# Kernel tuning notes

Measured on AMD Instinct MI355X. Metric: run time of the kernel, lower is better.

## Reference

```python
import jax, jax.numpy as jnp
import numpy as np

B, D, V, T = 256, 1024, 32000, 64  # num_seqs, hidden dim, vocab, history len


def setup_inputs() -> dict:
    key = jax.random.key(0)
    ks = jax.random.split(key, 8)
    hidden = jax.random.normal(ks[0], (B, D), dtype=jnp.float32)
    embedding = jax.random.normal(ks[1], (V, D), dtype=jnp.float32) * (1.0 / np.sqrt(D))
    output_tokens = jax.random.randint(ks[2], (B, T), 0, V, dtype=jnp.int64)
    presence_penalties = jax.random.uniform(ks[3], (B,), dtype=jnp.float32)
    frequency_penalties = jax.random.uniform(ks[4], (B,), dtype=jnp.float32)
    temperatures = jax.random.uniform(ks[5], (B,), dtype=jnp.float32) + 0.5  # > eps
    top_ps = jax.random.uniform(ks[6], (B,), dtype=jnp.float32) * 0.5 + 0.5  # in [0.5, 1.0)
    top_ks = jax.random.randint(ks[7], (B,), 1, V, dtype=jnp.int64)
    return {
        "hidden": hidden,
        "embedding": embedding,
        "output_tokens": output_tokens,
        "presence_penalties": presence_penalties,
        "frequency_penalties": frequency_penalties,
        "temperatures": temperatures,
        "top_ps": top_ps,
        "top_ks": top_ks,
    }


def reference(hidden, embedding, output_tokens, presence_penalties,
              frequency_penalties, temperatures, top_ps, top_ks):
    # 1) logits = pruned hidden states @ embedding^T  -> [B, V]
    logits = jnp.einsum("bd,vd->bv", hidden, embedding)
    b, v = logits.shape

    # 2) presence/frequency penalties via per-row token histogram (np.bincount equiv)
    rows = jnp.broadcast_to(jnp.arange(b)[:, None], output_tokens.shape)
    counts = jnp.zeros((b, v), logits.dtype).at[rows, output_tokens].add(1.0)
    logits = logits - frequency_penalties[:, None] * counts \
                    - presence_penalties[:, None] * (counts > 0).astype(logits.dtype)

    # 3) temperature scaling
    logits = logits / temperatures[:, None]

    # 4) probabilities
    probs = jax.nn.softmax(logits, axis=-1)

    # 5) top-p / top-k: descending sort, cumsum masks, scatter back via inverse perm
    order = jnp.argsort(-probs, axis=-1)                       # descending order
    probs_sort = jnp.take_along_axis(probs, order, axis=-1)
    probs_cum = jnp.cumsum(probs_sort, axis=-1)
    top_p_mask = (probs_cum - probs_sort) > top_ps[:, None]
    top_k_mask = jnp.arange(v)[None, :] >= top_ks[:, None]
    probs_sort = jnp.where(top_p_mask | top_k_mask, 0.0, probs_sort)
    inv = jnp.argsort(order, axis=-1)
    filtered_probs = jnp.take_along_axis(probs_sort, inv, axis=-1)  # original order
    return filtered_probs
```

## Files before the change

kernel.cpp:

```cpp
#include <hip/hip_runtime.h>
#include <math.h>

#define NB 256
#define NV 32000
#define ND 1024
#define NT 64

#define GN 64
#define ASTR 56
#define NKB 64
#define ASLAB (256 * ASTR)
#define NGBLK (NV / GN)
#define INV2048F 4.8828125e-4f

#define NBIN 1024
#define FIX2 4294967296.0
#define PACK1 (1ull << 48)
#define SMASK ((1ull << 48) - 1ull)
#define SMEM_BYTES (NV * 4 + NBIN * 8)

typedef _Float16 f16x8 __attribute__((ext_vector_type(8)));
typedef _Float16 f16x4 __attribute__((ext_vector_type(4)));
typedef float f32x16 __attribute__((ext_vector_type(16)));
typedef __attribute__((address_space(3))) void lds_void;
typedef __attribute__((address_space(1))) void glb_void;

struct RowP2 {
  unsigned long long basePack;
  unsigned long long toppZfix;
  unsigned pfx;
  int ktop;
  float invZ;
  unsigned ustar;
  int m;
  int cEq;
};

__device__ __forceinline__ unsigned mono_enc(float f) {
  unsigned u = __float_as_uint(f);
  return (u & 0x80000000u) ? ~u : (u | 0x80000000u);
}
__device__ __forceinline__ float mono_dec(unsigned u) {
  return (u & 0x80000000u) ? __uint_as_float(u & 0x7FFFFFFFu) : __uint_as_float(~u);
}

__global__ __launch_bounds__(256) void convert_A(const float* __restrict__ hidden,
                                                 _Float16* __restrict__ A3) {
  const int kb = blockIdx.x, t = threadIdx.x;
  __shared__ _Float16 slab[ASLAB];
#pragma unroll
  for (int it = 0; it < 4; it++) {
    const int m = it * 64 + (t >> 2);
    const int k4 = (t & 3) * 4;
    float4 a4 = *(const float4*)(hidden + (size_t)m * ND + kb * 16 + k4);
    _Float16* base = slab + m * ASTR;
    float v[4] = {a4.x, a4.y, a4.z, a4.w};
#pragma unroll
    for (int q = 0; q < 4; q++) {
      const _Float16 h = (_Float16)v[q];
      const _Float16 l2 = (_Float16)((v[q] - (float)h) * 2048.0f);
      const int kk = k4 + q;
      base[kk] = h;
      base[16 + 2 * kk] = h;
      base[17 + 2 * kk] = l2;
    }
  }
  __syncthreads();
  const uint4* s = (const uint4*)slab;
  uint4* g = (uint4*)(A3 + (size_t)kb * ASLAB);
#pragma unroll
  for (int i = 0; i < 7; i++) g[i * 256 + t] = s[i * 256 + t];
}

__global__ __launch_bounds__(256, 2) void gemm_f16s(
    const float* __restrict__ Bm, const _Float16* __restrict__ A3,
    const float* __restrict__ temp, unsigned* __restrict__ rowmax,
    float* __restrict__ C) {
  __shared__ _Float16 Als[2][ASLAB];
  __shared__ _Float16 Bls[2][GN * ASTR];
  __shared__ float s_invT[256];
  __shared__ unsigned s_pm[256];

  const int t = threadIdx.x;
  const int l = t & 63, w = t >> 6;
  const int n0 = blockIdx.x * GN;
  s_invT[t] = 1.0f / temp[t];
  s_pm[t] = 0u;

  f32x16 accA[2][2] = {};
  f32x16 accB[2][2] = {};

  const int bn = t >> 2, bk4 = (t & 3) * 4;
  const int l31 = l & 31, lh = l >> 5;
  const int ka = lh * 8;
  const int mb = w * 64;

  const float* browp = Bm + (size_t)(n0 + bn) * ND + bk4;
  const char* gaBase = (const char*)A3 + (w * 7) * 1024 + l * 16;
  char* laB0 = (char*)&Als[0][0] + (w * 7) * 1024;
  char* laB1 = (char*)&Als[1][0] + (w * 7) * 1024;

#define ISSUE_A(kbn, LA)                                                        \
  do {                                                                          \
    const char* ga_ = gaBase + (size_t)(kbn) * (ASLAB * 2);                     \
    _Pragma("unroll") for (int i_ = 0; i_ < 7; i_++)                            \
        __builtin_amdgcn_global_load_lds((const glb_void*)(ga_ + i_ * 1024),    \
                                         (lds_void*)((LA) + i_ * 1024), 16, 0,  \
                                         0);                                    \
  } while (0)

#define BCONV(BV, DST)                                                          \
  do {                                                                          \
    const _Float16 h0_ = (_Float16)(BV).x, h1_ = (_Float16)(BV).y,              \
                   h2_ = (_Float16)(BV).z, h3_ = (_Float16)(BV).w;              \
    const _Float16 q0_ = (_Float16)(((BV).x - (float)h0_) * 2048.0f);           \
    const _Float16 q1_ = (_Float16)(((BV).y - (float)h1_) * 2048.0f);           \
    const _Float16 q2_ = (_Float16)(((BV).z - (float)h2_) * 2048.0f);           \
    const _Float16 q3_ = (_Float16)(((BV).w - (float)h3_) * 2048.0f);           \
    _Float16* prow_ = (DST) + bn * ASTR;                                        \
    *(f16x4*)(prow_ + bk4) = (f16x4){h0_, h1_, h2_, h3_};                       \
    *(f16x8*)(prow_ + 16 + 2 * bk4) =                                           \
        (f16x8){q0_, h0_, q1_, h1_, q2_, h2_, q3_, h3_};                        \
  } while (0)

#define COMPUTE(CUR)                                                                       \
  do {                                                                                     \
    const _Float16* Ap_ = &Als[CUR][0] + (size_t)(mb + l31) * ASTR + ka;                   \
    const _Float16* Bp_ = &Bls[CUR][0] + (size_t)l31 * ASTR + ka;                          \
    f16x8 a0_ = *(const f16x8*)(Ap_);                                                      \
    f16x8 a1_ = *(const f16x8*)(Ap_ + 32 * ASTR);                                          \
    f16x8 b0_ = *(const f16x8*)(Bp_);                                                      \
    f16x8 b1_ = *(const f16x8*)(Bp_ + 32 * ASTR);                                          \
    accA[0][0] = __builtin_amdgcn_mfma_f32_32x32x16_f16(a0_, b0_, accA[0][0], 0, 0, 0);    \
    accA[0][1] = __builtin_amdgcn_mfma_f32_32x32x16_f16(a0_, b1_, accA[0][1], 0, 0, 0);    \
    accA[1][0] = __builtin_amdgcn_mfma_f32_32x32x16_f16(a1_, b0_, accA[1][0], 0, 0, 0);    \
    accA[1][1] = __builtin_amdgcn_mfma_f32_32x32x16_f16(a1_, b1_, accA[1][1], 0, 0, 0);    \
    _Pragma("unroll") for (int s_ = 0; s_ < 2; s_++) {                                     \
      const int off_ = 16 + s_ * 16;                                                       \
      f16x8 c0_ = *(const f16x8*)(Ap_ + off_);                                             \
      f16x8 c1_ = *(const f16x8*)(Ap_ + 32 * ASTR + off_);                                 \
      f16x8 d0_ = *(const f16x8*)(Bp_ + off_);                                             \
      f16x8 d1_ = *(const f16x8*)(Bp_ + 32 * ASTR + off_);                                 \
      accB[0][0] = __builtin_amdgcn_mfma_f32_32x32x16_f16(c0_, d0_, accB[0][0], 0, 0, 0);  \
      accB[0][1] = __builtin_amdgcn_mfma_f32_32x32x16_f16(c0_, d1_, accB[0][1], 0, 0, 0);  \
      accB[1][0] = __builtin_amdgcn_mfma_f32_32x32x16_f16(c1_, d0_, accB[1][0], 0, 0, 0);  \
      accB[1][1] = __builtin_amdgcn_mfma_f32_32x32x16_f16(c1_, d1_, accB[1][1], 0, 0, 0);  \
    }                                                                                      \
  } while (0)

  ISSUE_A(0, laB0);
  __builtin_amdgcn_sched_barrier(0);
  float4 bv0 = *(const float4*)(browp);
  __builtin_amdgcn_sched_barrier(0);
  float4 bvA = *(const float4*)(browp + 16);
  __builtin_amdgcn_sched_barrier(0);
  asm volatile("s_waitcnt vmcnt(1)" ::: "memory");
  BCONV(bv0, &Bls[0][0]);
  asm volatile("s_waitcnt lgkmcnt(0)\ns_barrier" ::: "memory");

  float4 bvB;
  for (int kb = 0; kb < 62; kb += 2) {
    ISSUE_A(kb + 1, laB1);
    __builtin_amdgcn_sched_barrier(0);
    bvB = *(const float4*)(browp + (size_t)(kb + 2) * 16);
    __builtin_amdgcn_sched_barrier(0);
    asm volatile("s_waitcnt vmcnt(9)" ::: "memory");
    COMPUTE(0);
    __builtin_amdgcn_sched_barrier(0);
    asm volatile("s_waitcnt vmcnt(8)" ::: "memory");
    BCONV(bvA, &Bls[1][0]);
    asm volatile("s_waitcnt lgkmcnt(0)\ns_barrier" ::: "memory");

    ISSUE_A(kb + 2, laB0);
    __builtin_amdgcn_sched_barrier(0);
    bvA = *(const float4*)(browp + (size_t)(kb + 3) * 16);
    __builtin_amdgcn_sched_barrier(0);
    asm volatile("s_waitcnt vmcnt(9)" ::: "memory");
    COMPUTE(1);
    __builtin_amdgcn_sched_barrier(0);
    asm volatile("s_waitcnt vmcnt(8)" ::: "memory");
    BCONV(bvB, &Bls[0][0]);
    asm volatile("s_waitcnt lgkmcnt(0)\ns_barrier" ::: "memory");
  }

  ISSUE_A(63, laB1);
  __builtin_amdgcn_sched_barrier(0);
  asm volatile("s_waitcnt vmcnt(8)" ::: "memory");
  COMPUTE(0);
  __builtin_amdgcn_sched_barrier(0);
  asm volatile("s_waitcnt vmcnt(7)" ::: "memory");
  BCONV(bvA, &Bls[1][0]);
  asm volatile("s_waitcnt lgkmcnt(0)\ns_barrier" ::: "memory");

  asm volatile("s_waitcnt vmcnt(0)" ::: "memory");
  COMPUTE(1);

#undef ISSUE_A
#undef BCONV
#undef COMPUTE

#pragma unroll
  for (int mi = 0; mi < 2; mi++) {
#pragma unroll
    for (int r = 0; r < 16; r++) {
      const int row = mb + mi * 32 + (r & 3) + 8 * (r >> 2) + 4 * lh;
      const float it = s_invT[row];
      float v0 = (accA[mi][0][r] + accB[mi][0][r] * INV2048F) * it;
      float v1 = (accA[mi][1][r] + accB[mi][1][r] * INV2048F) * it;
      C[(size_t)row * NV + n0 + l31] = v0;
      C[(size_t)row * NV + n0 + 32 + l31] = v1;
      float mx = fmaxf(v0, v1);
#pragma unroll
      for (int o = 1; o < 32; o <<= 1) mx = fmaxf(mx, __shfl_xor(mx, o));
      if (l31 == 0) atomicMax(&s_pm[row], mono_enc(mx));
    }
  }
  __syncthreads();
  atomicMax(&rowmax[t], s_pm[t]);
}

__global__ __launch_bounds__(256) void sample_row(
    float* __restrict__ buf, const unsigned* __restrict__ rowmax,
    const int* __restrict__ toks, const float* __restrict__ pres,
    const float* __restrict__ freq, const float* __restrict__ temp,
    const float* __restrict__ topp_a, const int* __restrict__ topk_a) {
  extern __shared__ char smem[];
  float* e = (float*)smem;
  unsigned long long* h = (unsigned long long*)(smem + NV * 4);
  __shared__ unsigned long long sc[256];
  __shared__ int s_rank[256];
  __shared__ int s_tok[NT];
  __shared__ int s_bs;
  __shared__ RowP2 sp;

  const int b = blockIdx.x, t = threadIdx.x;
  float* row = buf + (size_t)b * NV;

  if (t < NT) s_tok[t] = toks[b * NT + t];
  for (int i = t; i < NBIN; i += 256) h[i] = 0ull;
  for (int i4 = t; i4 < NV / 4; i4 += 256)
    *(float4*)(e + i4 * 4) = *(const float4*)(row + i4 * 4);
  __syncthreads();

  if (t < NT) {
    const int tk = s_tok[t];
    bool first = true; int cnt = 0;
    for (int j = 0; j < NT; j++)
      if (s_tok[j] == tk) { if (j < t) first = false; cnt++; }
    if (first) e[tk] -= (freq[b] * (float)cnt + pres[b]) / temp[b];
  }
  __syncthreads();

  const float M = mono_dec(rowmax[b]);
  for (int i4 = t; i4 < NV / 4; i4 += 256) {
    float4 x4 = *(const float4*)(e + i4 * 4);
    float4 e4;
    e4.x = expf(x4.x - M); e4.y = expf(x4.y - M);
    e4.z = expf(x4.z - M); e4.w = expf(x4.w - M);
    *(float4*)(e + i4 * 4) = e4;
    unsigned k;
    k = __float_as_uint(e4.x); if (k) atomicAdd(&h[k >> 20], PACK1 | (unsigned long long)(e4.x * FIX2));
    k = __float_as_uint(e4.y); if (k) atomicAdd(&h[k >> 20], PACK1 | (unsigned long long)(e4.y * FIX2));
    k = __float_as_uint(e4.z); if (k) atomicAdd(&h[k >> 20], PACK1 | (unsigned long long)(e4.z * FIX2));
    k = __float_as_uint(e4.w); if (k) atomicAdd(&h[k >> 20], PACK1 | (unsigned long long)(e4.w * FIX2));
  }
  __syncthreads();

  for (int level = 0; level < 3; level++) {
    unsigned long long v0 = h[t * 4], v1 = h[t * 4 + 1],
                       v2 = h[t * 4 + 2], v3 = h[t * 4 + 3];
    if (t == 0) s_bs = 1023;
    sc[t] = v0 + v1 + v2 + v3;
    __syncthreads();
    for (int off = 1; off < 256; off <<= 1) {
      unsigned long long add = (t + off < 256) ? sc[t + off] : 0ull;
      __syncthreads();
      sc[t] += add;
      __syncthreads();
    }
    const unsigned long long totalP = sc[0];
    unsigned long long run = (t < 255) ? sc[t + 1] : 0ull;
    h[t * 4 + 3] = run; run += v3;
    h[t * 4 + 2] = run; run += v2;
    h[t * 4 + 1] = run; run += v1;
    h[t * 4 + 0] = run;
    __syncthreads();

    unsigned long long base, toppZ;
    int ktop_;
    if (level == 0) {
      ktop_ = topk_a[b];
      unsigned long long Zfix = totalP & SMASK;
      if (!Zfix) Zfix = 1ull;
      toppZ = (unsigned long long)((double)topp_a[b] * (double)Zfix);
      base = 0ull;
    } else {
      base = sp.basePack; toppZ = sp.toppZfix; ktop_ = sp.ktop;
    }

#pragma unroll
    for (int i = 0; i < 4; i++) {
      const int bin = t * 4 + i;
      const unsigned long long sG = base + h[bin];
      const bool A = ((long long)(sG >> 48) < (long long)ktop_) && ((sG & SMASK) <= toppZ);
      const unsigned long long sPfull = base + ((bin > 0) ? h[bin - 1] : totalP);
      const bool Ap = ((long long)(sPfull >> 48) < (long long)ktop_) && ((sPfull & SMASK) <= toppZ);
      if (A && !Ap) s_bs = bin;
    }
    __syncthreads();
    if (t == 0) {
      const int bs = s_bs;
      const unsigned long long newBase = base + h[bs];
      if (level == 0) {
        unsigned long long Zfix = totalP & SMASK;
        if (!Zfix) Zfix = 1ull;
        sp.invZ = (float)(FIX2 / (double)Zfix);
      }
      if (level < 2) {
        sp.basePack = newBase;
        sp.toppZfix = toppZ;
        sp.ktop = ktop_;
        sp.pfx = (level == 0) ? (unsigned)bs : ((sp.pfx << 10) | (unsigned)bs);
      } else {
        const unsigned ustar = (sp.pfx << 10) | (unsigned)bs;
        const unsigned long long raw = ((bs > 0) ? h[bs - 1] : totalP) - h[bs];
        const int cEq = (int)(raw >> 48);
        const long long Chi = (long long)(newBase >> 48);
        const unsigned long long Shi = newBase & SMASK;
        long long m = cEq;
        const long long lim = (long long)ktop_ - Chi;
        if (lim < m) m = lim;
        const double tf = (double)__uint_as_float(ustar) * FIX2;
        const double rem = (double)(toppZ - Shi);
        const double Rd = floor(rem / tf) + 1.0;
        if (Rd < (double)m) m = (long long)Rd;
        if (m < 1) m = 1;
        sp.ustar = ustar; sp.m = (int)m; sp.cEq = cEq;
      }
    }
    __syncthreads();
    if (level < 2) {
      for (int i = t; i < NBIN; i += 256) h[i] = 0ull;
      __syncthreads();
      const unsigned pfx = sp.pfx;
      const int ms = (level == 0) ? 20 : 10;
      const int bsh = (level == 0) ? 10 : 0;
      for (int i4 = t; i4 < NV / 4; i4 += 256) {
        float4 e4 = *(const float4*)(e + i4 * 4);
        unsigned k;
        k = __float_as_uint(e4.x); if (k && (k >> ms) == pfx) atomicAdd(&h[(k >> bsh) & 1023u], PACK1 | (unsigned long long)(e4.x * FIX2));
        k = __float_as_uint(e4.y); if (k && (k >> ms) == pfx) atomicAdd(&h[(k >> bsh) & 1023u], PACK1 | (unsigned long long)(e4.y * FIX2));
        k = __float_as_uint(e4.z); if (k && (k >> ms) == pfx) atomicAdd(&h[(k >> bsh) & 1023u], PACK1 | (unsigned long long)(e4.z * FIX2));
        k = __float_as_uint(e4.w); if (k && (k >> ms) == pfx) atomicAdd(&h[(k >> bsh) & 1023u], PACK1 | (unsigned long long)(e4.w * FIX2));
      }
      __syncthreads();
    }
  }

  const unsigned ustar = sp.ustar;
  const float invZ = sp.invZ;
  if (sp.m >= sp.cEq) {
    for (int i4 = t; i4 < NV / 4; i4 += 256) {
      float4 e4 = *(const float4*)(e + i4 * 4);
      float4 o4;
      unsigned k;
      k = __float_as_uint(e4.x); o4.x = (k >= ustar) ? e4.x * invZ : 0.f;
      k = __float_as_uint(e4.y); o4.y = (k >= ustar) ? e4.y * invZ : 0.f;
      k = __float_as_uint(e4.z); o4.z = (k >= ustar) ? e4.z * invZ : 0.f;
      k = __float_as_uint(e4.w); o4.w = (k >= ustar) ? e4.w * invZ : 0.f;
      *(float4*)(row + i4 * 4) = o4;
    }
  } else {
    const int m = sp.m;
    const int CH = NV / 256;
    const int base0 = t * CH;
    int myc = 0;
    for (int v = base0; v < base0 + CH; v++)
      myc += (__float_as_uint(e[v]) == ustar);
    s_rank[t] = myc;
    __syncthreads();
    for (int off = 1; off < 256; off <<= 1) {
      const int a0 = s_rank[t];
      const int an = (t >= off) ? s_rank[t - off] : 0;
      __syncthreads();
      s_rank[t] = a0 + an;
      __syncthreads();
    }
    int r = (t > 0) ? s_rank[t - 1] : 0;
    for (int v = base0; v < base0 + CH; v++) {
      const unsigned k = __float_as_uint(e[v]);
      float o = (k > ustar) ? e[v] * invZ : 0.f;
      if (k == ustar) { o = (r < m) ? e[v] * invZ : 0.f; r++; }
      row[v] = o;
    }
  }
}

extern "C" void kernel_launch(void* const* d_in, const int* in_sizes, int n_in,
                              void* d_out, int out_size, void* d_ws, size_t ws_size,
                              hipStream_t stream) {
  (void)in_sizes; (void)n_in; (void)out_size; (void)ws_size;
  const float* hidden = (const float*)d_in[0];
  const float* emb    = (const float*)d_in[1];
  const int*   toks   = (const int*)d_in[2];
  const float* pres   = (const float*)d_in[3];
  const float* freq   = (const float*)d_in[4];
  const float* temp   = (const float*)d_in[5];
  const float* topp   = (const float*)d_in[6];
  const int*   topk   = (const int*)d_in[7];
  float* out = (float*)d_out;

  const size_t offA3 = 0;
  const size_t offRM = 1835008;

  _Float16* A3 = (_Float16*)((char*)d_ws + offA3);
  unsigned* rowmax = (unsigned*)((char*)d_ws + offRM);

  hipFuncSetAttribute((const void*)sample_row,
                      hipFuncAttributeMaxDynamicSharedMemorySize, SMEM_BYTES);

  hipMemsetAsync((char*)d_ws + offRM, 0, 1024, stream);
  convert_A<<<NKB, 256, 0, stream>>>(hidden, A3);
  gemm_f16s<<<NGBLK, 256, 0, stream>>>(emb, A3, temp, rowmax, out);
  sample_row<<<NB, 256, SMEM_BYTES, stream>>>(out, rowmax, toks, pres, freq,
                                              temp, topp, topk);
}
```

Baseline: 324.2 us.

## Widen sampling kernel to 1024 threads with split 32-bit privatized histograms

The per-row sampling kernel now runs with 1024 threads instead of 256. The 64-bit packed LDS atomics for the radix-select histogram are replaced by pairs of 32-bit atomics (a low word plus a combined high/carry/count word), spread over two privatized copies chosen by wavefront parity. The scan now has one bin per thread, and the tie-rank scan is widened to 1024. This aims to cut the cost of 64-bit LDS atomic contention and to add parallelism per row, at the cost of two atomics per element, longer barrier-bound scans, and lower occupancy per CU.

```diff
diff --git a/kernel.cpp b/kernel.cpp
--- a/kernel.cpp
+++ b/kernel.cpp
@@ -14,10 +14,11 @@
 #define INV2048F 4.8828125e-4f
 
 #define NBIN 1024
+#define HSTR 1032
+#define HTOT (4 * HSTR)
 #define FIX2 4294967296.0
-#define PACK1 (1ull << 48)
 #define SMASK ((1ull << 48) - 1ull)
-#define SMEM_BYTES (NV * 4 + NBIN * 8)
+#define SMEM_BYTES (NV * 4 + HTOT * 4)
 
 typedef _Float16 f16x8 __attribute__((ext_vector_type(8)));
 typedef _Float16 f16x4 __attribute__((ext_vector_type(4)));
@@ -219,26 +220,38 @@
   atomicMax(&rowmax[t], s_pm[t]);
 }
 
-__global__ __launch_bounds__(256) void sample_row(
+__global__ __launch_bounds__(1024) void sample_row(
     float* __restrict__ buf, const unsigned* __restrict__ rowmax,
     const int* __restrict__ toks, const float* __restrict__ pres,
     const float* __restrict__ freq, const float* __restrict__ temp,
     const float* __restrict__ topp_a, const int* __restrict__ topk_a) {
   extern __shared__ char smem[];
   float* e = (float*)smem;
-  unsigned long long* h = (unsigned long long*)(smem + NV * 4);
-  __shared__ unsigned long long sc[256];
-  __shared__ int s_rank[256];
+  unsigned* hist = (unsigned*)(smem + NV * 4);
+  unsigned long long* suf = (unsigned long long*)hist;
   __shared__ int s_tok[NT];
   __shared__ int s_bs;
   __shared__ RowP2 sp;
 
   const int b = blockIdx.x, t = threadIdx.x;
+  const int cp = (t >> 6) & 1;
+  unsigned* loP = hist + cp * HSTR;
+  unsigned* hcP = hist + 2 * HSTR + cp * HSTR;
   float* row = buf + (size_t)b * NV;
 
+#define HACC(EV, BIN)                                                    \
+  do {                                                                   \
+    unsigned long long f_ = (unsigned long long)((double)(EV) * FIX2);   \
+    unsigned flo_ = (unsigned)f_;                                        \
+    unsigned old_ = atomicAdd(&loP[BIN], flo_);                          \
+    unsigned hc_ = 0x10000u + (unsigned)(f_ >> 32) +                     \
+                   ((old_ + flo_ < flo_) ? 1u : 0u);                     \
+    atomicAdd(&hcP[BIN], hc_);                                           \
+  } while (0)
+
   if (t < NT) s_tok[t] = toks[b * NT + t];
-  for (int i = t; i < NBIN; i += 256) h[i] = 0ull;
-  for (int i4 = t; i4 < NV / 4; i4 += 256)
+  for (int i = t; i < HTOT; i += 1024) hist[i] = 0u;
+  for (int i4 = t; i4 < NV / 4; i4 += 1024)
     *(float4*)(e + i4 * 4) = *(const float4*)(row + i4 * 4);
   __syncthreads();
 
@@ -252,38 +265,39 @@
   __syncthreads();
 
   const float M = mono_dec(rowmax[b]);
-  for (int i4 = t; i4 < NV / 4; i4 += 256) {
+  for (int i4 = t; i4 < NV / 4; i4 += 1024) {
     float4 x4 = *(const float4*)(e + i4 * 4);
     float4 e4;
     e4.x = expf(x4.x - M); e4.y = expf(x4.y - M);
     e4.z = expf(x4.z - M); e4.w = expf(x4.w - M);
     *(float4*)(e + i4 * 4) = e4;
     unsigned k;
-    k = __float_as_uint(e4.x); if (k) atomicAdd(&h[k >> 20], PACK1 | (unsigned long long)(e4.x * FIX2));
-    k = __float_as_uint(e4.y); if (k) atomicAdd(&h[k >> 20], PACK1 | (unsigned long long)(e4.y * FIX2));
-    k = __float_as_uint(e4.z); if (k) atomicAdd(&h[k >> 20], PACK1 | (unsigned long long)(e4.z * FIX2));
-    k = __float_as_uint(e4.w); if (k) atomicAdd(&h[k >> 20], PACK1 | (unsigned long long)(e4.w * FIX2));
+    k = __float_as_uint(e4.x); if (k) HACC(e4.x, k >> 20);
+    k = __float_as_uint(e4.y); if (k) HACC(e4.y, k >> 20);
+    k = __float_as_uint(e4.z); if (k) HACC(e4.z, k >> 20);
+    k = __float_as_uint(e4.w); if (k) HACC(e4.w, k >> 20);
   }
   __syncthreads();
 
   for (int level = 0; level < 3; level++) {
-    unsigned long long v0 = h[t * 4], v1 = h[t * 4 + 1],
-                       v2 = h[t * 4 + 2], v3 = h[t * 4 + 3];
-    if (t == 0) s_bs = 1023;
-    sc[t] = v0 + v1 + v2 + v3;
-    __syncthreads();
-    for (int off = 1; off < 256; off <<= 1) {
-      unsigned long long add = (t + off < 256) ? sc[t + off] : 0ull;
-      __syncthreads();
-      sc[t] += add;
-      __syncthreads();
-    }
-    const unsigned long long totalP = sc[0];
-    unsigned long long run = (t < 255) ? sc[t + 1] : 0ull;
-    h[t * 4 + 3] = run; run += v3;
-    h[t * 4 + 2] = run; run += v2;
-    h[t * 4 + 1] = run; run += v1;
-    h[t * 4 + 0] = run;
+    const unsigned lo0 = hist[t], lo1 = hist[HSTR + t];
+    const unsigned hc0 = hist[2 * HSTR + t], hc1 = hist[3 * HSTR + t];
+    const unsigned c = (hc0 >> 16) + (hc1 >> 16);
+    const unsigned long long sum =
+        (((unsigned long long)((hc0 & 0xFFFFu) + (hc1 & 0xFFFFu))) << 32) +
+        (unsigned long long)lo0 + (unsigned long long)lo1;
+    const unsigned long long v = ((unsigned long long)c << 48) + sum;
+    __syncthreads();
+    suf[t] = v;
+    __syncthreads();
+    for (int off = 1; off < NBIN; off <<= 1) {
+      unsigned long long add = (t + off < NBIN) ? suf[t + off] : 0ull;
+      __syncthreads();
+      suf[t] += add;
+      __syncthreads();
+    }
+    const unsigned long long totalP = suf[0];
+    if (t == 0) s_bs = NBIN - 1;
     __syncthreads();
 
     unsigned long long base, toppZ;
@@ -298,19 +312,17 @@
       base = sp.basePack; toppZ = sp.toppZfix; ktop_ = sp.ktop;
     }
 
-#pragma unroll
-    for (int i = 0; i < 4; i++) {
-      const int bin = t * 4 + i;
-      const unsigned long long sG = base + h[bin];
+    {
+      const unsigned long long sG = base + suf[t];
       const bool A = ((long long)(sG >> 48) < (long long)ktop_) && ((sG & SMASK) <= toppZ);
-      const unsigned long long sPfull = base + ((bin > 0) ? h[bin - 1] : totalP);
-      const bool Ap = ((long long)(sPfull >> 48) < (long long)ktop_) && ((sPfull & SMASK) <= toppZ);
-      if (A && !Ap) s_bs = bin;
+      const unsigned long long sP = base + ((t > 0) ? suf[t - 1] : totalP);
+      const bool Ap = ((long long)(sP >> 48) < (long long)ktop_) && ((sP & SMASK) <= toppZ);
+      if (A && !Ap) s_bs = t;
     }
     __syncthreads();
     if (t == 0) {
       const int bs = s_bs;
-      const unsigned long long newBase = base + h[bs];
+      const unsigned long long newBase = base + suf[bs];
       if (level == 0) {
         unsigned long long Zfix = totalP & SMASK;
         if (!Zfix) Zfix = 1ull;
@@ -323,7 +335,7 @@
         sp.pfx = (level == 0) ? (unsigned)bs : ((sp.pfx << 10) | (unsigned)bs);
       } else {
         const unsigned ustar = (sp.pfx << 10) | (unsigned)bs;
-        const unsigned long long raw = ((bs > 0) ? h[bs - 1] : totalP) - h[bs];
+        const unsigned long long raw = ((bs > 0) ? suf[bs - 1] : totalP) - suf[bs];
         const int cEq = (int)(raw >> 48);
         const long long Chi = (long long)(newBase >> 48);
         const unsigned long long Shi = newBase & SMASK;
@@ -339,28 +351,30 @@
       }
     }
     __syncthreads();
+
     if (level < 2) {
-      for (int i = t; i < NBIN; i += 256) h[i] = 0ull;
+      for (int i = t; i < HTOT; i += 1024) hist[i] = 0u;
       __syncthreads();
       const unsigned pfx = sp.pfx;
       const int ms = (level == 0) ? 20 : 10;
       const int bsh = (level == 0) ? 10 : 0;
-      for (int i4 = t; i4 < NV / 4; i4 += 256) {
+      for (int i4 = t; i4 < NV / 4; i4 += 1024) {
         float4 e4 = *(const float4*)(e + i4 * 4);
         unsigned k;
-        k = __float_as_uint(e4.x); if (k && (k >> ms) == pfx) atomicAdd(&h[(k >> bsh) & 1023u], PACK1 | (unsigned long long)(e4.x * FIX2));
-        k = __float_as_uint(e4.y); if (k && (k >> ms) == pfx) atomicAdd(&h[(k >> bsh) & 1023u], PACK1 | (unsigned long long)(e4.y * FIX2));
-        k = __float_as_uint(e4.z); if (k && (k >> ms) == pfx) atomicAdd(&h[(k >> bsh) & 1023u], PACK1 | (unsigned long long)(e4.z * FIX2));
-        k = __float_as_uint(e4.w); if (k && (k >> ms) == pfx) atomicAdd(&h[(k >> bsh) & 1023u], PACK1 | (unsigned long long)(e4.w * FIX2));
+        k = __float_as_uint(e4.x); if (k && (k >> ms) == pfx) HACC(e4.x, (k >> bsh) & 1023u);
+        k = __float_as_uint(e4.y); if (k && (k >> ms) == pfx) HACC(e4.y, (k >> bsh) & 1023u);
+        k = __float_as_uint(e4.z); if (k && (k >> ms) == pfx) HACC(e4.z, (k >> bsh) & 1023u);
+        k = __float_as_uint(e4.w); if (k && (k >> ms) == pfx) HACC(e4.w, (k >> bsh) & 1023u);
       }
       __syncthreads();
     }
   }
+#undef HACC
 
   const unsigned ustar = sp.ustar;
   const float invZ = sp.invZ;
   if (sp.m >= sp.cEq) {
-    for (int i4 = t; i4 < NV / 4; i4 += 256) {
+    for (int i4 = t; i4 < NV / 4; i4 += 1024) {
       float4 e4 = *(const float4*)(e + i4 * 4);
       float4 o4;
       unsigned k;
@@ -372,22 +386,23 @@
     }
   } else {
     const int m = sp.m;
-    const int CH = NV / 256;
-    const int base0 = t * CH;
+    unsigned* rk = hist;
+    const int base0 = t * 32;
+    const int end0 = (base0 + 32 < NV) ? base0 + 32 : NV;
     int myc = 0;
-    for (int v = base0; v < base0 + CH; v++)
+    for (int v = base0; v < end0; v++)
       myc += (__float_as_uint(e[v]) == ustar);
-    s_rank[t] = myc;
-    __syncthreads();
-    for (int off = 1; off < 256; off <<= 1) {
-      const int a0 = s_rank[t];
-      const int an = (t >= off) ? s_rank[t - off] : 0;
-      __syncthreads();
-      s_rank[t] = a0 + an;
-      __syncthreads();
-    }
-    int r = (t > 0) ? s_rank[t - 1] : 0;
-    for (int v = base0; v < base0 + CH; v++) {
+    rk[t] = (unsigned)myc;
+    __syncthreads();
+    for (int off = 1; off < 1024; off <<= 1) {
+      const unsigned a0 = rk[t];
+      const unsigned an = (t >= off) ? rk[t - off] : 0u;
+      __syncthreads();
+      rk[t] = a0 + an;
+      __syncthreads();
+    }
+    int r = (t > 0) ? (int)rk[t - 1] : 0;
+    for (int v = base0; v < end0; v++) {
       const unsigned k = __float_as_uint(e[v]);
       float o = (k > ustar) ? e[v] * invZ : 0.f;
       if (k == ustar) { o = (r < m) ? e[v] * invZ : 0.f; r++; }
@@ -422,6 +437,6 @@
   hipMemsetAsync((char*)d_ws + offRM, 0, 1024, stream);
   convert_A<<<NKB, 256, 0, stream>>>(hidden, A3);
   gemm_f16s<<<NGBLK, 256, 0, stream>>>(emb, A3, temp, rowmax, out);
-  sample_row<<<NB, 256, SMEM_BYTES, stream>>>(out, rowmax, toks, pres, freq,
-                                              temp, topp, topk);
-}
+  sample_row<<<NB, 1024, SMEM_BYTES, stream>>>(out, rowmax, toks, pres, freq,
+                                               temp, topp, topk);
+}
```

Result: faster. 300.0 us (-7.5%).
